# Performance work log

Measured on AMD Instinct MI355X. Metric: run time of the kernel, lower is better.

Reference implementation:

```python
import jax, jax.numpy as jnp
import numpy as np
import math

N = 262144
POS_FREQ = 6
TIME_FREQ = 10
HIDDEN = 256
POS_ENC_DIM = 3 + 3 * 2 * POS_FREQ      # 39
TIME_ENC_DIM = 1 + 1 * 2 * TIME_FREQ    # 21
INPUT_DIM = POS_ENC_DIM + TIME_ENC_DIM  # 60
SKIP_LAYER = 2


def sin_enc(x, num_freqs):
    # x: (..., D) -> (..., D + D*2*L)
    freqs = (2.0 ** jnp.arange(num_freqs, dtype=jnp.float32)) * math.pi  # (L,)
    scaled = x[..., None] * freqs                       # (..., D, L)
    enc = jnp.concatenate([jnp.sin(scaled), jnp.cos(scaled)], axis=-1)  # (..., D, 2L)
    enc = enc.reshape(*x.shape[:-1], -1)                # (..., D*2L)
    return jnp.concatenate([x, enc], axis=-1)


def setup_inputs() -> dict:
    key = jax.random.key(0)
    ks = jax.random.split(key, 20)
    canonical_xyz = jax.random.normal(ks[0], (N, 3), dtype=jnp.float32)
    time = jax.random.uniform(ks[1], (1, 1), dtype=jnp.float32)

    def linear(k, in_dim, out_dim, std=None):
        kw, kb = jax.random.split(k)
        if std is None:
            bound = 1.0 / np.sqrt(in_dim)
            W = jax.random.uniform(kw, (out_dim, in_dim), minval=-bound, maxval=bound, dtype=jnp.float32)
            b = jax.random.uniform(kb, (out_dim,), minval=-bound, maxval=bound, dtype=jnp.float32)
        else:
            W = jax.random.normal(kw, (out_dim, in_dim), dtype=jnp.float32) * std
            b = jnp.zeros((out_dim,), dtype=jnp.float32)
        return W, b

    W0, b0 = linear(ks[2], INPUT_DIM, HIDDEN)
    W1, b1 = linear(ks[3], HIDDEN, HIDDEN)
    W2, b2 = linear(ks[4], HIDDEN + INPUT_DIM, HIDDEN)  # skip layer
    W3, b3 = linear(ks[5], HIDDEN, HIDDEN)
    Wxyz, bxyz = linear(ks[6], HIDDEN, 3, std=1e-4)
    Wrot, brot = linear(ks[7], HIDDEN, 4, std=1e-4)
    Wscale, bscale = linear(ks[8], HIDDEN, 3, std=1e-4)
    Wop, bop = linear(ks[9], HIDDEN, 1, std=1e-4)
    return {
        'canonical_xyz': canonical_xyz, 'time': time,
        'W0': W0, 'b0': b0, 'W1': W1, 'b1': b1, 'W2': W2, 'b2': b2, 'W3': W3, 'b3': b3,
        'Wxyz': Wxyz, 'bxyz': bxyz, 'Wrot': Wrot, 'brot': brot,
        'Wscale': Wscale, 'bscale': bscale, 'Wop': Wop, 'bop': bop,
    }


def reference(canonical_xyz, time, W0, b0, W1, b1, W2, b2, W3, b3,
              Wxyz, bxyz, Wrot, brot, Wscale, bscale, Wop, bop):
    n = canonical_xyz.shape[0]
    time_encoded = jnp.broadcast_to(sin_enc(time.reshape(1, 1), TIME_FREQ), (n, TIME_ENC_DIM))
    pos_encoded = sin_enc(canonical_xyz, POS_FREQ)          # (N, 39)
    x_input = jnp.concatenate([pos_encoded, time_encoded], axis=-1)  # (N, 60)

    h = x_input
    Ws = [W0, W1, W2, W3]
    bs = [b0, b1, b2, b3]
    for i in range(4):
        if i == SKIP_LAYER:
            h = jnp.concatenate([h, x_input], axis=-1)
        h = jax.nn.relu(h @ Ws[i].T + bs[i])

    delta_xyz = h @ Wxyz.T + bxyz
    delta_rotation = h @ Wrot.T + brot
    delta_scaling = h @ Wscale.T + bscale
    delta_opacity = h @ Wop.T + bop
    return (delta_xyz, delta_rotation, delta_scaling, delta_opacity)
```

## Files before the change

### kernel.cpp

```cpp
#include <hip/hip_runtime.h>
#include <math.h>

typedef _Float16 half8 __attribute__((ext_vector_type(8)));
typedef _Float16 half4 __attribute__((ext_vector_type(4)));
typedef float f32x4 __attribute__((ext_vector_type(4)));

#define NPTS 262144
#define BM 128
#define NTHREADS 512

#define CHUNK_SHORTS 16384
#define WH_OFF (14 * CHUNK_SHORTS)

typedef const __attribute__((address_space(1))) void g_void_t;
typedef __attribute__((address_space(3))) void l_void_t;

__device__ __forceinline__ short f2h(float f) {
  _Float16 h = (_Float16)f;
  return __builtin_bit_cast(short, h);
}

__global__ void prep_kernel(const float* __restrict__ W0, const float* __restrict__ W1,
                            const float* __restrict__ W2, const float* __restrict__ W3,
                            const float* __restrict__ Wxyz, const float* __restrict__ Wrot,
                            const float* __restrict__ Wscale, const float* __restrict__ Wop,
                            short* __restrict__ ws) {
  const int stride = gridDim.x * blockDim.x;
  const int t0 = blockIdx.x * blockDim.x + threadIdx.x;
  for (int i = t0; i < 14 * CHUNK_SHORTS; i += stride) {
    const int c = i >> 14;
    const int r = (i >> 6) & 255;
    const int kk = i & 63;
    float v = 0.0f;
    if (c == 0)      { if (kk < 60) v = W0[r * 60 + kk]; }
    else if (c <= 4) { v = W1[r * 256 + (c - 1) * 64 + kk]; }
    else if (c <= 8) { v = W2[r * 316 + (c - 5) * 64 + kk]; }
    else if (c == 9) { if (kk < 60) v = W2[r * 316 + 256 + kk]; }
    else             { v = W3[r * 256 + (c - 10) * 64 + kk]; }
    ws[c * CHUNK_SHORTS + r * 64 + (kk ^ ((r & 7) << 3))] = f2h(v);
  }
  for (int i = t0; i < 16 * 256; i += stride) {
    const int j = i >> 8, k = i & 255;
    float v = 0.0f;
    if (j < 3) v = Wxyz[j * 256 + k];
    else if (j < 7) v = Wrot[(j - 3) * 256 + k];
    else if (j < 10) v = Wscale[(j - 7) * 256 + k];
    else if (j == 10) v = Wop[k];
    ws[WH_OFF + i] = f2h(v);
  }
}

__device__ __forceinline__ void stage_chunk(const short* __restrict__ ws, int c,
                                            short* dst, int t) {
  const char* src = (const char*)(ws + c * CHUNK_SHORTS);
  char* d = (char*)dst;
  const int wave = t >> 6;
  const int lane = t & 63;
#pragma unroll
  for (int r = 0; r < 4; ++r) {
    const int off = r * 8192 + wave * 1024;
    __builtin_amdgcn_global_load_lds((g_void_t*)(src + off + lane * 16),
                                     (l_void_t*)(d + off), 16, 0, 0);
  }
}

__device__ __forceinline__ void compute_chunk(f32x4 (&acc)[4][4],
                                              const short* wb,
                                              const char* bsrc, int bstride, int bkbase,
                                              int fg, int pg, int lr, int lk) {
  half8 a[2][4], b[2][4];
#pragma unroll
  for (int ks = 0; ks < 2; ++ks) {
#pragma unroll
    for (int x = 0; x < 4; ++x) {
      const int row = fg * 64 + x * 16 + lr;
      a[ks][x] = *(const half8*)((const char*)wb + row * 128 +
                                 ((ks * 64 + lk * 16) ^ ((row & 7) << 4)));
      const int m = pg * 64 + x * 16 + lr;
      b[ks][x] = *(const half8*)(bsrc + m * bstride +
                                 ((bkbase + ks * 64 + lk * 16) ^ ((m & 7) << 4)));
    }
  }
#pragma unroll
  for (int ks = 0; ks < 2; ++ks)
#pragma unroll
    for (int jt = 0; jt < 4; ++jt)
#pragma unroll
      for (int mt = 0; mt < 4; ++mt)
        acc[jt][mt] = __builtin_amdgcn_mfma_f32_16x16x32_f16(a[ks][jt], b[ks][mt],
                                                             acc[jt][mt], 0, 0, 0);
}

__device__ __forceinline__ void zero_acc(f32x4 (&acc)[4][4]) {
#pragma unroll
  for (int jt = 0; jt < 4; ++jt)
#pragma unroll
    for (int mt = 0; mt < 4; ++mt) {
      f32x4 z = {0.f, 0.f, 0.f, 0.f};
      acc[jt][mt] = z;
    }
}

__device__ __forceinline__ void epilogue(f32x4 (&acc)[4][4], const float* __restrict__ bias,
                                         char* dst, int fg, int pg, int lr, int lk) {
#pragma unroll
  for (int jt = 0; jt < 4; ++jt) {
    const int j0 = fg * 64 + jt * 16 + lk * 4;
    const f32x4 bv = *(const f32x4*)(bias + j0);
#pragma unroll
    for (int mt = 0; mt < 4; ++mt) {
      const int m = pg * 64 + mt * 16 + lr;
      half4 hv;
#pragma unroll
      for (int r = 0; r < 4; ++r) hv[r] = (_Float16)fmaxf(acc[jt][mt][r] + bv[r], 0.f);
      *(half4*)(dst + ((m * 512 + j0 * 2) ^ ((m & 7) << 4))) = hv;
    }
  }
}

__global__ __launch_bounds__(NTHREADS, 2) void deform_kernel(
    const float* __restrict__ xyz, const float* __restrict__ tptr,
    const float* __restrict__ b0, const float* __restrict__ b1,
    const float* __restrict__ b2, const float* __restrict__ b3,
    const float* __restrict__ bxyz, const float* __restrict__ brot,
    const float* __restrict__ bscale, const float* __restrict__ bop,
    const short* __restrict__ ws, float* __restrict__ out) {
  __shared__ short xin[BM * 64];
  __shared__ short hbuf[BM * 256];
  __shared__ short wbuf[2][CHUNK_SHORTS];

  const int t = threadIdx.x;
  const int lane = t & 63;
  const int wid = t >> 6;
  const int fg = wid & 3;
  const int pg = wid >> 2;
  const int lr = lane & 15;
  const int lk = lane >> 4;
  const int p0 = blockIdx.x * BM;

  const float tval = tptr[0];

  {
    const int m = t >> 2, q = t & 3;
    const int p = p0 + m;
    const float xc[3] = {xyz[p * 3 + 0], xyz[p * 3 + 1], xyz[p * 3 + 2]};
    half8 v0, v1;
#pragma unroll
    for (int dd = 0; dd < 16; ++dd) {
      const int d = q * 16 + dd;
      float v;
      if (d < 3) {
        v = xc[d];
      } else if (d < 39) {
        const int idx = d - 3;
        const int c = idx / 12;
        const int r = idx - c * 12;
        const int e = (r >= 6) ? r - 6 : r;
        const float rev = xc[c] * (0.5f * (float)(1 << e));
        const float fr = rev - floorf(rev);
        v = (r < 6) ? __builtin_amdgcn_sinf(fr) : __builtin_amdgcn_cosf(fr);
      } else if (d == 39) {
        v = tval;
      } else if (d < 60) {
        const int r = d - 40;
        const int e = (r >= 10) ? r - 10 : r;
        const float rev = tval * (0.5f * (float)(1 << e));
        const float fr = rev - floorf(rev);
        v = (r < 10) ? __builtin_amdgcn_sinf(fr) : __builtin_amdgcn_cosf(fr);
      } else {
        v = 0.f;
      }
      const _Float16 hv = (_Float16)v;
      if (dd < 8) v0[dd] = hv; else v1[dd - 8] = hv;
    }
    char* base = (char*)xin;
    *(half8*)(base + ((m * 128 + q * 32) ^ ((m & 7) << 4))) = v0;
    *(half8*)(base + ((m * 128 + q * 32 + 16) ^ ((m & 7) << 4))) = v1;
  }

  stage_chunk(ws, 0, wbuf[0], t);
  __syncthreads();

  f32x4 acc[4][4];
  zero_acc(acc);

#define CHUNK_STEP(c, bsrc, bstride, bkbase)                                   \
  {                                                                            \
    if ((c) + 1 < 14) stage_chunk(ws, (c) + 1, wbuf[((c) + 1) & 1], t);        \
    compute_chunk(acc, wbuf[(c) & 1], bsrc, bstride, bkbase, fg, pg, lr, lk);  \
    __syncthreads();                                                           \
  }

  CHUNK_STEP(0, (const char*)xin, 128, 0);
  epilogue(acc, b0, (char*)hbuf, fg, pg, lr, lk);
  zero_acc(acc);
  __syncthreads();

  CHUNK_STEP(1, (const char*)hbuf, 512, 0);
  CHUNK_STEP(2, (const char*)hbuf, 512, 128);
  CHUNK_STEP(3, (const char*)hbuf, 512, 256);
  CHUNK_STEP(4, (const char*)hbuf, 512, 384);
  epilogue(acc, b1, (char*)hbuf, fg, pg, lr, lk);
  zero_acc(acc);
  __syncthreads();

  CHUNK_STEP(5, (const char*)hbuf, 512, 0);
  CHUNK_STEP(6, (const char*)hbuf, 512, 128);
  CHUNK_STEP(7, (const char*)hbuf, 512, 256);
  CHUNK_STEP(8, (const char*)hbuf, 512, 384);
  CHUNK_STEP(9, (const char*)xin, 128, 0);
  epilogue(acc, b2, (char*)hbuf, fg, pg, lr, lk);
  zero_acc(acc);
  __syncthreads();

  CHUNK_STEP(10, (const char*)hbuf, 512, 0);
  CHUNK_STEP(11, (const char*)hbuf, 512, 128);
  CHUNK_STEP(12, (const char*)hbuf, 512, 256);
  CHUNK_STEP(13, (const char*)hbuf, 512, 384);
  epilogue(acc, b3, (char*)hbuf, fg, pg, lr, lk);
  __syncthreads();
#undef CHUNK_STEP

  if (fg == 0) {
    f32x4 hacc[4];
#pragma unroll
    for (int mt = 0; mt < 4; ++mt) {
      f32x4 z = {0.f, 0.f, 0.f, 0.f};
      hacc[mt] = z;
    }
    const short* WH = ws + WH_OFF;
#pragma unroll
    for (int ks = 0; ks < 8; ++ks) {
      const half8 ah = *(const half8*)(WH + lr * 256 + ks * 32 + lk * 8);
#pragma unroll
      for (int mt = 0; mt < 4; ++mt) {
        const int m = pg * 64 + mt * 16 + lr;
        const half8 bh = *(const half8*)((const char*)hbuf +
                                         ((m * 512 + ks * 64 + lk * 16) ^ ((m & 7) << 4)));
        hacc[mt] = __builtin_amdgcn_mfma_f32_16x16x32_f16(ah, bh, hacc[mt], 0, 0, 0);
      }
    }
    float hb[4];
#pragma unroll
    for (int r = 0; r < 4; ++r) {
      const int j = lk * 4 + r;
      hb[r] = (j < 3) ? bxyz[j] : (j < 7) ? brot[j - 3] : (j < 10) ? bscale[j - 7]
              : (j == 10) ? bop[0] : 0.f;
    }
#pragma unroll
    for (int mt = 0; mt < 4; ++mt) {
      const int p = p0 + pg * 64 + mt * 16 + lr;
#pragma unroll
      for (int r = 0; r < 4; ++r) {
        const int j = lk * 4 + r;
        const float v = hacc[mt][r] + hb[r];
        if (j < 3)        out[p * 3 + j] = v;
        else if (j < 7)   out[3 * NPTS + p * 4 + (j - 3)] = v;
        else if (j < 10)  out[7 * NPTS + p * 3 + (j - 7)] = v;
        else if (j == 10) out[10 * NPTS + p] = v;
      }
    }
  }
}

extern "C" void kernel_launch(void* const* d_in, const int* in_sizes, int n_in,
                              void* d_out, int out_size, void* d_ws, size_t ws_size,
                              hipStream_t stream) {
  const float* xyz    = (const float*)d_in[0];
  const float* tptr   = (const float*)d_in[1];
  const float* W0     = (const float*)d_in[2];
  const float* b0     = (const float*)d_in[3];
  const float* W1     = (const float*)d_in[4];
  const float* b1     = (const float*)d_in[5];
  const float* W2     = (const float*)d_in[6];
  const float* b2     = (const float*)d_in[7];
  const float* W3     = (const float*)d_in[8];
  const float* b3     = (const float*)d_in[9];
  const float* Wxyz   = (const float*)d_in[10];
  const float* bxyz   = (const float*)d_in[11];
  const float* Wrot   = (const float*)d_in[12];
  const float* brot   = (const float*)d_in[13];
  const float* Wscale = (const float*)d_in[14];
  const float* bscale = (const float*)d_in[15];
  const float* Wop    = (const float*)d_in[16];
  const float* bop    = (const float*)d_in[17];
  short* ws  = (short*)d_ws;
  float* out = (float*)d_out;

  prep_kernel<<<256, 256, 0, stream>>>(W0, W1, W2, W3, Wxyz, Wrot, Wscale, Wop, ws);
  deform_kernel<<<NPTS / BM, NTHREADS, 0, stream>>>(xyz, tptr, b0, b1, b2, b3,
                                                    bxyz, brot, bscale, bop, ws, out);
}
```

Before: 246.2 us.

## Load weight fragments directly from global into registers, dropping LDS weight staging

The prep kernel now writes weights in MFMA fragment order, so each wave can load its A fragments straight from global/L2 into registers with coalesced 16-byte loads. The LDS double buffer for weights and the per-chunk barriers are removed. Register double-buffering (aA/aB) prefetches the next chunk's fragments during the current MFMAs. This frees LDS and cuts synchronisation, but adds register pressure and makes every wave fetch weights from cache on its own.

Measured after the change: 280.5 us. 13.9% more time.

```diff
diff --git a/kernel.cpp b/kernel.cpp
--- a/kernel.cpp
+++ b/kernel.cpp
@@ -11,9 +11,6 @@
 
 #define CHUNK_SHORTS 16384
 #define WH_OFF (14 * CHUNK_SHORTS)
-
-typedef const __attribute__((address_space(1))) void g_void_t;
-typedef __attribute__((address_space(3))) void l_void_t;
 
 __device__ __forceinline__ short f2h(float f) {
   _Float16 h = (_Float16)f;
@@ -29,15 +26,20 @@
   const int t0 = blockIdx.x * blockDim.x + threadIdx.x;
   for (int i = t0; i < 14 * CHUNK_SHORTS; i += stride) {
     const int c = i >> 14;
-    const int r = (i >> 6) & 255;
-    const int kk = i & 63;
+    const int q = i & 16383;
+    const int rb = q >> 10;
+    const int kb = (q >> 9) & 1;
+    const int lane = (q >> 3) & 63;
+    const int e = q & 7;
+    const int r = rb * 16 + (lane & 15);
+    const int kk = kb * 32 + (lane >> 4) * 8 + e;
     float v = 0.0f;
     if (c == 0)      { if (kk < 60) v = W0[r * 60 + kk]; }
     else if (c <= 4) { v = W1[r * 256 + (c - 1) * 64 + kk]; }
     else if (c <= 8) { v = W2[r * 316 + (c - 5) * 64 + kk]; }
     else if (c == 9) { if (kk < 60) v = W2[r * 316 + 256 + kk]; }
     else             { v = W3[r * 256 + (c - 10) * 64 + kk]; }
-    ws[c * CHUNK_SHORTS + r * 64 + (kk ^ ((r & 7) << 3))] = f2h(v);
+    ws[i] = f2h(v);
   }
   for (int i = t0; i < 16 * 256; i += stride) {
     const int j = i >> 8, k = i & 255;
@@ -50,44 +52,41 @@
   }
 }
 
-__device__ __forceinline__ void stage_chunk(const short* __restrict__ ws, int c,
-                                            short* dst, int t) {
-  const char* src = (const char*)(ws + c * CHUNK_SHORTS);
-  char* d = (char*)dst;
-  const int wave = t >> 6;
-  const int lane = t & 63;
-#pragma unroll
-  for (int r = 0; r < 4; ++r) {
-    const int off = r * 8192 + wave * 1024;
-    __builtin_amdgcn_global_load_lds((g_void_t*)(src + off + lane * 16),
-                                     (l_void_t*)(d + off), 16, 0, 0);
-  }
-}
-
-__device__ __forceinline__ void compute_chunk(f32x4 (&acc)[4][4],
-                                              const short* wb,
-                                              const char* bsrc, int bstride, int bkbase,
-                                              int fg, int pg, int lr, int lk) {
-  half8 a[2][4], b[2][4];
-#pragma unroll
-  for (int ks = 0; ks < 2; ++ks) {
-#pragma unroll
-    for (int x = 0; x < 4; ++x) {
-      const int row = fg * 64 + x * 16 + lr;
-      a[ks][x] = *(const half8*)((const char*)wb + row * 128 +
-                                 ((ks * 64 + lk * 16) ^ ((row & 7) << 4)));
+__device__ __forceinline__ void load_afrags(half8 (&dst)[8], const short* __restrict__ ws,
+                                            int c, int fg, int lane) {
+  const short* base = ws + c * CHUNK_SHORTS + fg * 4096 + lane * 8;
+#pragma unroll
+  for (int f = 0; f < 8; ++f) dst[f] = *(const half8*)(base + f * 512);
+}
+
+__device__ __forceinline__ void load_bfrags(half8 (&b)[8], const char* bsrc, int bstride,
+                                            int bkbase, int pg, int lr, int lk) {
+#pragma unroll
+  for (int x = 0; x < 4; ++x)
+#pragma unroll
+    for (int ks = 0; ks < 2; ++ks) {
       const int m = pg * 64 + x * 16 + lr;
-      b[ks][x] = *(const half8*)(bsrc + m * bstride +
-                                 ((bkbase + ks * 64 + lk * 16) ^ ((m & 7) << 4)));
-    }
-  }
+      b[x * 2 + ks] = *(const half8*)(bsrc + m * bstride +
+                                      ((bkbase + ks * 64 + lk * 16) ^ ((m & 7) << 4)));
+    }
+}
+
+__device__ __forceinline__ void chunk_step(f32x4 (&acc)[4][4], half8 (&acur)[8],
+                                           half8 (&anxt)[8], bool prefetch, int cnext,
+                                           const short* __restrict__ ws,
+                                           const char* bsrc, int bstride, int bkbase,
+                                           int fg, int pg, int lr, int lk, int lane) {
+  if (prefetch) load_afrags(anxt, ws, cnext, fg, lane);
+  half8 bf[8];
+  load_bfrags(bf, bsrc, bstride, bkbase, pg, lr, lk);
 #pragma unroll
   for (int ks = 0; ks < 2; ++ks)
 #pragma unroll
     for (int jt = 0; jt < 4; ++jt)
 #pragma unroll
       for (int mt = 0; mt < 4; ++mt)
-        acc[jt][mt] = __builtin_amdgcn_mfma_f32_16x16x32_f16(a[ks][jt], b[ks][mt],
+        acc[jt][mt] = __builtin_amdgcn_mfma_f32_16x16x32_f16(acur[jt * 2 + ks],
+                                                             bf[mt * 2 + ks],
                                                              acc[jt][mt], 0, 0, 0);
 }
 
@@ -125,9 +124,8 @@
     const float* __restrict__ bxyz, const float* __restrict__ brot,
     const float* __restrict__ bscale, const float* __restrict__ bop,
     const short* __restrict__ ws, float* __restrict__ out) {
-  __shared__ short xin[BM * 64];
-  __shared__ short hbuf[BM * 256];
-  __shared__ short wbuf[2][CHUNK_SHORTS];
+  __shared__ __align__(16) short xin[BM * 64];
+  __shared__ __align__(16) short hbuf[BM * 256];
 
   const int t = threadIdx.x;
   const int lane = t & 63;
@@ -137,6 +135,9 @@
   const int lr = lane & 15;
   const int lk = lane >> 4;
   const int p0 = blockIdx.x * BM;
+
+  half8 aA[8], aB[8];
+  load_afrags(aA, ws, 0, fg, lane);
 
   const float tval = tptr[0];
 
@@ -177,49 +178,42 @@
     *(half8*)(base + ((m * 128 + q * 32) ^ ((m & 7) << 4))) = v0;
     *(half8*)(base + ((m * 128 + q * 32 + 16) ^ ((m & 7) << 4))) = v1;
   }
-
-  stage_chunk(ws, 0, wbuf[0], t);
   __syncthreads();
 
   f32x4 acc[4][4];
   zero_acc(acc);
 
-#define CHUNK_STEP(c, bsrc, bstride, bkbase)                                   \
-  {                                                                            \
-    if ((c) + 1 < 14) stage_chunk(ws, (c) + 1, wbuf[((c) + 1) & 1], t);        \
-    compute_chunk(acc, wbuf[(c) & 1], bsrc, bstride, bkbase, fg, pg, lr, lk);  \
-    __syncthreads();                                                           \
-  }
-
-  CHUNK_STEP(0, (const char*)xin, 128, 0);
+  chunk_step(acc, aA, aB, true, 1, ws, (const char*)xin, 128, 0, fg, pg, lr, lk, lane);
   epilogue(acc, b0, (char*)hbuf, fg, pg, lr, lk);
   zero_acc(acc);
   __syncthreads();
 
-  CHUNK_STEP(1, (const char*)hbuf, 512, 0);
-  CHUNK_STEP(2, (const char*)hbuf, 512, 128);
-  CHUNK_STEP(3, (const char*)hbuf, 512, 256);
-  CHUNK_STEP(4, (const char*)hbuf, 512, 384);
+  chunk_step(acc, aB, aA, true, 2, ws, (const char*)hbuf, 512, 0,   fg, pg, lr, lk, lane);
+  chunk_step(acc, aA, aB, true, 3, ws, (const char*)hbuf, 512, 128, fg, pg, lr, lk, lane);
+  chunk_step(acc, aB, aA, true, 4, ws, (const char*)hbuf, 512, 256, fg, pg, lr, lk, lane);
+  chunk_step(acc, aA, aB, true, 5, ws, (const char*)hbuf, 512, 384, fg, pg, lr, lk, lane);
+  __syncthreads();
   epilogue(acc, b1, (char*)hbuf, fg, pg, lr, lk);
   zero_acc(acc);
   __syncthreads();
 
-  CHUNK_STEP(5, (const char*)hbuf, 512, 0);
-  CHUNK_STEP(6, (const char*)hbuf, 512, 128);
-  CHUNK_STEP(7, (const char*)hbuf, 512, 256);
-  CHUNK_STEP(8, (const char*)hbuf, 512, 384);
-  CHUNK_STEP(9, (const char*)xin, 128, 0);
+  chunk_step(acc, aB, aA, true, 6, ws, (const char*)hbuf, 512, 0,   fg, pg, lr, lk, lane);
+  chunk_step(acc, aA, aB, true, 7, ws, (const char*)hbuf, 512, 128, fg, pg, lr, lk, lane);
+  chunk_step(acc, aB, aA, true, 8, ws, (const char*)hbuf, 512, 256, fg, pg, lr, lk, lane);
+  chunk_step(acc, aA, aB, true, 9, ws, (const char*)hbuf, 512, 384, fg, pg, lr, lk, lane);
+  chunk_step(acc, aB, aA, true, 10, ws, (const char*)xin, 128, 0,   fg, pg, lr, lk, lane);
+  __syncthreads();
   epilogue(acc, b2, (char*)hbuf, fg, pg, lr, lk);
   zero_acc(acc);
   __syncthreads();
 
-  CHUNK_STEP(10, (const char*)hbuf, 512, 0);
-  CHUNK_STEP(11, (const char*)hbuf, 512, 128);
-  CHUNK_STEP(12, (const char*)hbuf, 512, 256);
-  CHUNK_STEP(13, (const char*)hbuf, 512, 384);
+  chunk_step(acc, aA, aB, true, 11, ws, (const char*)hbuf, 512, 0,   fg, pg, lr, lk, lane);
+  chunk_step(acc, aB, aA, true, 12, ws, (const char*)hbuf, 512, 128, fg, pg, lr, lk, lane);
+  chunk_step(acc, aA, aB, true, 13, ws, (const char*)hbuf, 512, 256, fg, pg, lr, lk, lane);
+  chunk_step(acc, aB, aA, false, 0, ws, (const char*)hbuf, 512, 384, fg, pg, lr, lk, lane);
+  __syncthreads();
   epilogue(acc, b3, (char*)hbuf, fg, pg, lr, lk);
   __syncthreads();
-#undef CHUNK_STEP
 
   if (fg == 0) {
     f32x4 hacc[4];
```
